# Kernel optimization log

Hardware: AMD Instinct MI355X
Metric: run time of the kernel (lower is better)

## Reference

```python
import jax, jax.numpy as jnp
import numpy as np

NGRAM_NS = (2, 3)  # window sizes of the 2 hidden layers ('2,3,4' -> num_hidden_layers=2)


def _ngram(x, n):
    # x: (b, s, d) -> (b, s, n, d); window i holds x[i:i+n], zero-padded at the end
    s = x.shape[1]
    xp = jnp.pad(x, ((0, 0), (0, n - 1), (0, 0)))
    return jnp.stack([xp[:, j:j + s] for j in range(n)], axis=2)


def _mixture_weighted(r, i, w):
    # r,i: (..., n, d); w: (..., n, 1) -> weighted sum of outer products |phi><phi|
    w = w[..., 0]
    Rr = jnp.einsum('...nd,...ne,...n->...de', r, r, w) + jnp.einsum('...nd,...ne,...n->...de', i, i, w)
    Ri = jnp.einsum('...nd,...ne,...n->...de', i, r, w) - jnp.einsum('...nd,...ne,...n->...de', r, i, w)
    return Rr, Ri


def _normalize_complex(vr, vi):
    n = jnp.sqrt(jnp.sum(vr * vr + vi * vi, axis=-1, keepdims=True))
    return vr / n, vi / n


def _quad_form(Rr, Ri, vr, vi):
    # <v_k| rho |v_k> for each measurement vector v_k; Rr,Ri: (..., d, d); vr,vi: (k, d)
    ar = jnp.einsum('...de,ke->...dk', Rr, vr) - jnp.einsum('...de,ke->...dk', Ri, vi)
    ai = jnp.einsum('...de,ke->...dk', Rr, vi) + jnp.einsum('...de,ke->...dk', Ri, vr)
    out_r = jnp.einsum('kd,...dk->...k', vr, ar) + jnp.einsum('kd,...dk->...k', vi, ai)
    out_i = jnp.einsum('kd,...dk->...k', vr, ai) - jnp.einsum('kd,...dk->...k', vi, ar)
    return out_r, out_i


def setup_inputs() -> dict:
    key = jax.random.key(0)
    ks = jax.random.split(key, 9)
    V, D, B, S, U, L = 50000, 100, 16, 128, 100, 2
    return {
        'input_seq': jax.random.randint(ks[0], (B, S), 0, V),
        'amp_table': jax.random.normal(ks[1], (V, D), jnp.float32),
        'phase_table': jax.random.uniform(ks[2], (V, D), jnp.float32, -np.pi, np.pi),
        'proj_kernel_r': jax.random.normal(ks[3], (L, D, D), jnp.float32),
        'proj_kernel_i': jax.random.normal(ks[4], (L, D, D), jnp.float32),
        'meas_kernel_r': jax.random.normal(ks[5], (U, D), jnp.float32),
        'meas_kernel_i': jax.random.normal(ks[6], (U, D), jnp.float32),
        'dense_w': jax.random.normal(ks[7], (U, 2), jnp.float32) * 0.1,
        'dense_b': jnp.zeros((2,), jnp.float32),
    }


def reference(input_seq, amp_table, phase_table, proj_kernel_r, proj_kernel_i,
              meas_kernel_r, meas_kernel_i, dense_w, dense_b):
    # ComplexEmbedding
    amp = amp_table[input_seq]      # (b, s, d)
    phase = phase_table[input_seq]  # (b, s, d)
    # L2Norm / L2Normalization
    weights = jnp.linalg.norm(amp, axis=-1, keepdims=True)  # (b, s, 1)
    amp = amp / weights
    # ComplexMultiply: state = amp * e^{i phase}
    seq_r = amp * jnp.cos(phase)
    seq_i = amp * jnp.sin(phase)
    for li, n in enumerate(NGRAM_NS):
        gr = _ngram(seq_r, n)                                  # (b, s, n, d)
        gi = _ngram(seq_i, n)
        gw = jax.nn.softmax(_ngram(weights, n), axis=1)        # Softmax(dim=1) as in torch code
        Rr, Ri = _mixture_weighted(gr, gi, gw)                 # (b, s, d, d)
        vr, vi = _normalize_complex(proj_kernel_r[li], proj_kernel_i[li])
        seq_r, seq_i = _quad_form(Rr, Ri, vr, vi)              # (b, s, d)
    # Final mixture over the sequence dim with the raw L2-norm weights
    Rr, Ri = _mixture_weighted(seq_r, seq_i, weights)          # (b, d, d)
    vr, vi = _normalize_complex(meas_kernel_r, meas_kernel_i)
    probs, _ = _quad_form(Rr, Ri, vr, vi)                      # (b, units) real part of Tr(rho P_k)
    return probs @ dense_w + dense_b
```

## Files before the change

kernel.cpp:

```cpp
#include <hip/hip_runtime.h>
#include <math.h>

#define NB 16
#define SS 128
#define DD 100
#define KK 100
#define T_TILE 8
#define NTILES 16
#define NT 768

__device__ __forceinline__ float dot4(const float4 a, const float4 b) {
  return a.x * b.x + a.y * b.y + a.z * b.z + a.w * b.w;
}

template<int MODE, int CM, int NA, int NB2>
__device__ __forceinline__ void do_stage(
    const float* __restrict__ gvr, const float* __restrict__ gvi,
    const float4 (*__restrict__ xR)[25], const float4 (*__restrict__ xI)[25],
    float4 (*__restrict__ partl)[11][50],
    float2 (*__restrict__ nrmh)[50],
    float* __restrict__ mdst, float2* __restrict__ y3f,
    float* __restrict__ invvnU,
    const float* __restrict__ es, const float* __restrict__ sc,
    int df4, int pmaxF, int pmaxC,
    int k0, bool act, int g, int h, int t0)
{
  const float* vr0 = gvr + k0 * DD + 4 * df4;
  const float* vi0 = gvi + k0 * DD + 4 * df4;
  float acr[4][2] = {{0.f,0.f},{0.f,0.f},{0.f,0.f},{0.f,0.f}};
  float aci[4][2] = {{0.f,0.f},{0.f,0.f},{0.f,0.f},{0.f,0.f}};
  float n0 = 0.f, n1 = 0.f;

  {
    float4 V[NA][2][2];
#pragma unroll
    for (int j = 0; j < NA; ++j) {
      V[j][0][0] = *(const float4*)(vr0 + 4 * j);
      V[j][1][0] = *(const float4*)(vr0 + DD + 4 * j);
      V[j][0][1] = *(const float4*)(vi0 + 4 * j);
      V[j][1][1] = *(const float4*)(vi0 + DD + 4 * j);
    }
#pragma unroll
    for (int j = 0; j < NA; ++j) {
      n0 += dot4(V[j][0][0], V[j][0][0]) + dot4(V[j][0][1], V[j][0][1]);
      n1 += dot4(V[j][1][0], V[j][1][0]) + dot4(V[j][1][1], V[j][1][1]);
    }
#pragma unroll
    for (int e = 0; e < 4; ++e) {
      const int p = 4 * g + e;
      if (p <= pmaxF) {
        const float4* xrow  = &xR[p][df4];
        const float4* xirow = &xI[p][df4];
#pragma unroll
        for (int j = 0; j < NA; ++j) {
          const float4 xr = xrow[j];
          if (MODE == 0) {
            const float4 xi = xirow[j];
            acr[e][0] += dot4(V[j][0][0], xr) + dot4(V[j][0][1], xi);
            aci[e][0] += dot4(V[j][0][0], xi) - dot4(V[j][0][1], xr);
            acr[e][1] += dot4(V[j][1][0], xr) + dot4(V[j][1][1], xi);
            aci[e][1] += dot4(V[j][1][0], xi) - dot4(V[j][1][1], xr);
          } else {
            acr[e][0] += dot4(V[j][0][0], xr);
            aci[e][0] += dot4(V[j][0][1], xr);
            acr[e][1] += dot4(V[j][1][0], xr);
            aci[e][1] += dot4(V[j][1][1], xr);
          }
        }
      }
    }
  }
  {
    float4 V[NB2][2][2];
#pragma unroll
    for (int j = 0; j < NB2; ++j) {
      V[j][0][0] = *(const float4*)(vr0 + 4 * (NA + j));
      V[j][1][0] = *(const float4*)(vr0 + DD + 4 * (NA + j));
      V[j][0][1] = *(const float4*)(vi0 + 4 * (NA + j));
      V[j][1][1] = *(const float4*)(vi0 + DD + 4 * (NA + j));
    }
#pragma unroll
    for (int j = 0; j < NB2; ++j) {
      n0 += dot4(V[j][0][0], V[j][0][0]) + dot4(V[j][0][1], V[j][0][1]);
      n1 += dot4(V[j][1][0], V[j][1][0]) + dot4(V[j][1][1], V[j][1][1]);
    }
#pragma unroll
    for (int e = 0; e < 4; ++e) {
      const int p = 4 * g + e;
      if (p <= pmaxF) {
        const float4* xrow  = &xR[p][df4 + NA];
        const float4* xirow = &xI[p][df4 + NA];
#pragma unroll
        for (int j = 0; j < NB2; ++j) {
          const float4 xr = xrow[j];
          if (MODE == 0) {
            const float4 xi = xirow[j];
            acr[e][0] += dot4(V[j][0][0], xr) + dot4(V[j][0][1], xi);
            aci[e][0] += dot4(V[j][0][0], xi) - dot4(V[j][0][1], xr);
            acr[e][1] += dot4(V[j][1][0], xr) + dot4(V[j][1][1], xi);
            aci[e][1] += dot4(V[j][1][0], xi) - dot4(V[j][1][1], xr);
          } else {
            acr[e][0] += dot4(V[j][0][0], xr);
            aci[e][0] += dot4(V[j][0][1], xr);
            acr[e][1] += dot4(V[j][1][0], xr);
            aci[e][1] += dot4(V[j][1][1], xr);
          }
        }
      }
    }
  }

  const int kp = k0 >> 1;
  if (act) {
#pragma unroll
    for (int e = 0; e < 4; ++e) {
      const int p = 4 * g + e;
      if (p <= pmaxF)
        partl[h][p][kp] = make_float4(acr[e][0], aci[e][0], acr[e][1], aci[e][1]);
    }
    if (g == 0) nrmh[h][kp] = make_float2(n0, n1);
  }
  __syncthreads();

  if (h == 0 && act) {
    const float2 q0 = nrmh[0][kp], q1 = nrmh[1][kp], q2 = nrmh[2][kp], q3 = nrmh[3][kp];
    const float iv0 = 1.f / (q0.x + q1.x + q2.x + q3.x);
    const float iv1 = 1.f / (q0.y + q1.y + q2.y + q3.y);
#pragma unroll
    for (int e = 0; e < 4; ++e) {
      const int p = 4 * g + e;
      if (p <= pmaxC) {
        float4 s  = partl[0][p][kp];
        float4 b1 = partl[1][p][kp], b2 = partl[2][p][kp], b3 = partl[3][p][kp];
        s.x += b1.x + b2.x + b3.x;  s.y += b1.y + b2.y + b3.y;
        s.z += b1.z + b2.z + b3.z;  s.w += b1.w + b2.w + b3.w;
        if (CM == 1) {
          *(float2*)(mdst + p * 100 + k0) =
              make_float2((s.x * s.x + s.y * s.y) * iv0,
                          (s.z * s.z + s.w * s.w) * iv1);
        } else if (CM == 2) {
          float4 u  = partl[0][p + 1][kp];
          float4 c1 = partl[1][p + 1][kp], c2 = partl[2][p + 1][kp], c3 = partl[3][p + 1][kp];
          u.x += c1.x + c2.x + c3.x;  u.y += c1.y + c2.y + c3.y;
          u.z += c1.z + c2.z + c3.z;  u.w += c1.w + c2.w + c3.w;
          const int t = t0 + p;
          const float w0 = es[t] / sc[0];
          const float w1 = es[t + 1] / sc[1];
          const float r0 = w0 * s.x + w1 * u.x, i0 = w0 * s.y + w1 * u.y;
          const float r1 = w0 * s.z + w1 * u.z, i1 = w0 * s.w + w1 * u.w;
          *(float2*)(mdst + p * 100 + k0) =
              make_float2((r0 * r0 + i0 * i0) * iv0, (r1 * r1 + i1 * i1) * iv1);
        } else {
          *(float4*)(y3f + p * 100 + k0) = s;
        }
      }
    }
    if (CM == 3 && g == 0) { invvnU[k0] = iv0; invvnU[k0 + 1] = iv1; }
  }
  __syncthreads();
}

__global__ __launch_bounds__(NT, 3) void k_fused(
    const int* __restrict__ seq,
    const float* __restrict__ ampT, const float* __restrict__ phT,
    const float* __restrict__ pkr, const float* __restrict__ pki,
    const float* __restrict__ mkr, const float* __restrict__ mki,
    float* __restrict__ partg)
{
  __shared__ float4 xbR[11][25];
  __shared__ float4 xbI[11][25];
  __shared__ float4 partl[4][11][50];
  __shared__ float2 y3[10][100];
  __shared__ float2 nrmh[4][50];
  __shared__ float invvnU[KK];
  __shared__ float es[SS + 8];
  __shared__ float wnl[SS];
  __shared__ float redw[2];
  __shared__ float sc[3];

  const int tid  = threadIdx.x;
  const int lane = tid & 63;
  const int wid  = tid >> 6;
  const int h    = wid & 3;
  const int g    = wid >> 2;
  const bool act = lane < 50;
  const int kp   = act ? lane : 49;
  const int k0   = 2 * kp;
  const int df4  = (h == 0) ? 0 : 7 + 6 * (h - 1);
  const int bt   = blockIdx.x;
  const int b    = bt >> 4;
  const int t0   = (bt & 15) * T_TILE;
  const int sb   = b * SS;

  if (tid < 512) {
    const int t = tid >> 2, qq = tid & 3;
    const int row = seq[sb + t];
    const float* ap = ampT + (long)row * DD;
    float s = 0.f;
#pragma unroll
    for (int i = 0; i < 7; ++i) {
      const int j = qq + 4 * i;
      if (j < 25) {
        const float4 a = *(const float4*)(ap + 4 * j);
        s += a.x * a.x + a.y * a.y + a.z * a.z + a.w * a.w;
      }
    }
    s += __shfl_xor(s, 1);
    s += __shfl_xor(s, 2);
    if (qq == 0) { const float n = sqrtf(s); wnl[t] = n; es[t] = expf(n); }
  }
  if (tid >= 512 && tid < 520) es[SS + tid - 512] = 0.f;
  __syncthreads();

  if (tid < SS) {
    float v = es[tid];
#pragma unroll
    for (int m = 32; m; m >>= 1) v += __shfl_xor(v, m);
    if ((tid & 63) == 0) redw[tid >> 6] = v;
  }
  for (int e2 = tid; e2 < 11 * DD; e2 += NT) {
    const int p = e2 / DD, d = e2 - p * DD;
    const int t = t0 + p;
    float pr = 0.f, pi = 0.f;
    if (t < SS) {
      const int row = seq[sb + t];
      const float a  = ampT[(long)row * DD + d];
      const float ph = phT[(long)row * DD + d];
      float sv, cv; sincosf(ph, &sv, &cv);
      const float an = a / wnl[t];
      pr = an * cv; pi = an * sv;
    }
    ((float*)xbR)[p * 100 + d] = pr;
    ((float*)xbI)[p * 100 + d] = pi;
  }
  __syncthreads();
  if (tid == 0) {
    const float E = redw[0] + redw[1];
    sc[0] = E; sc[1] = E - es[0] + 1.f; sc[2] = E - es[0] - es[1] + 2.f;
  }
  __syncthreads();

  if (h == 0) do_stage<0,1,4,3>(pkr, pki, xbR, xbI, partl, nrmh,
                                (float*)xbR, nullptr, invvnU, es, sc,
                                0,   10, 10, k0, act, g, h, t0);
  else        do_stage<0,1,3,3>(pkr, pki, xbR, xbI, partl, nrmh,
                                (float*)xbR, nullptr, invvnU, es, sc,
                                df4, 10, 10, k0, act, g, h, t0);

  if (h == 0) do_stage<1,2,4,3>(pkr + DD * DD, pki + DD * DD, xbR, xbI, partl, nrmh,
                                (float*)xbI, nullptr, invvnU, es, sc,
                                0,   10, 9, k0, act, g, h, t0);
  else        do_stage<1,2,3,3>(pkr + DD * DD, pki + DD * DD, xbR, xbI, partl, nrmh,
                                (float*)xbI, nullptr, invvnU, es, sc,
                                df4, 10, 9, k0, act, g, h, t0);

  if (h == 0) do_stage<1,3,4,3>(mkr, mki, xbI, xbI, partl, nrmh,
                                nullptr, (float2*)y3, invvnU, es, sc,
                                0,   9, 9, k0, act, g, h, t0);
  else        do_stage<1,3,3,3>(mkr, mki, xbI, xbI, partl, nrmh,
                                nullptr, (float2*)y3, invvnU, es, sc,
                                df4, 9, 9, k0, act, g, h, t0);

  if (tid < KK) {
    const int k = tid;
    const float iE = 1.f / sc[0], iZ1 = 1.f / sc[1], iZ2 = 1.f / sc[2];
    float acc = 0.f;
#pragma unroll
    for (int p = 0; p < T_TILE; ++p) {
      const int t = t0 + p;
      const float w0 = es[t] * iE;
      const float w1 = es[t + 1] * iZ1;
      const float w2 = es[t + 2] * iZ2;
      const float2 a = y3[p][k], bb = y3[p + 1][k], c = y3[p + 2][k];
      const float qr = w0 * a.x + w1 * bb.x + w2 * c.x;
      const float qi = w0 * a.y + w1 * bb.y + w2 * c.y;
      acc += wnl[t] * (qr * qr + qi * qi);
    }
    partg[bt * KK + k] = acc * invvnU[k];
  }
}

__global__ __launch_bounds__(128) void k_out(
    const float* __restrict__ partg, const float* __restrict__ dw,
    const float* __restrict__ db, float* __restrict__ out)
{
  __shared__ float pr[KK];
  const int b = blockIdx.x, tid = threadIdx.x;
  if (tid < KK) {
    float s = 0.f;
#pragma unroll
    for (int q = 0; q < NTILES; ++q) s += partg[(b * NTILES + q) * KK + tid];
    pr[tid] = s;
  }
  __syncthreads();
  if (tid < 2) {
    float s = db[tid];
    for (int k = 0; k < KK; ++k) s += pr[k] * dw[k * 2 + tid];
    out[b * 2 + tid] = s;
  }
}

extern "C" void kernel_launch(void* const* d_in, const int* in_sizes, int n_in,
                              void* d_out, int out_size, void* d_ws, size_t ws_size,
                              hipStream_t stream) {
  const int*   seq  = (const int*)d_in[0];
  const float* ampT = (const float*)d_in[1];
  const float* phT  = (const float*)d_in[2];
  const float* pkr  = (const float*)d_in[3];
  const float* pki  = (const float*)d_in[4];
  const float* mkr  = (const float*)d_in[5];
  const float* mki  = (const float*)d_in[6];
  const float* dw   = (const float*)d_in[7];
  const float* db   = (const float*)d_in[8];
  float* out   = (float*)d_out;
  float* partg = (float*)d_ws;

  k_fused<<<NB * NTILES, NT, 0, stream>>>(seq, ampT, phT, pkr, pki, mkr, mki, partg);
  k_out  <<<NB,          128, 0, stream>>>(partg, dw, db, out);
}
```

Before: 37.85 us.

## Stage projection vectors via async global-to-LDS loads and split norm kernel

Projection and measurement vectors are now staged into shared memory with global_load_lds using a rotated layout, then read per thread, where before each thread loaded them directly from global memory. The per-sequence norm and softmax statistics move into a separate k_norm kernel, so each fused block no longer recomputes them. The block shrinks from 768 to 512 threads, with each wave group covering six positions instead of four. The change adds a kernel launch and extra barriers per stage, and the shared buffer is reused for partial sums.

```diff
diff --git a/kernel.cpp b/kernel.cpp
--- a/kernel.cpp
+++ b/kernel.cpp
@@ -7,175 +7,205 @@
 #define KK 100
 #define T_TILE 8
 #define NTILES 16
-#define NT 768
+#define NT 512
 
 __device__ __forceinline__ float dot4(const float4 a, const float4 b) {
   return a.x * b.x + a.y * b.y + a.z * b.z + a.w * b.w;
 }
 
-template<int MODE, int CM, int NA, int NB2>
+__device__ __forceinline__ int div25(int x) { return (x * 10486) >> 18; }
+
+__device__ __forceinline__ void stage_part(const float* __restrict__ gv,
+                                           char* vs, int wid, int lane) {
+#pragma unroll
+  for (int ii = 0; ii < 5; ++ii) {
+    const int i = wid + 8 * ii;
+    const int L = (i << 6) + lane;
+    const int k = div25(L);
+    const int s = L - 25 * k;
+    int t = s + 150 - 3 * (k >> 1);
+    t -= 25 * div25(t);
+    const float* src = gv + k * DD + 4 * t;
+    __builtin_amdgcn_global_load_lds(src, (float*)(vs + (i << 10)), 16, 0, 0);
+  }
+}
+
+template<int MODE, int CM>
 __device__ __forceinline__ void do_stage(
     const float* __restrict__ gvr, const float* __restrict__ gvi,
-    const float4 (*__restrict__ xR)[25], const float4 (*__restrict__ xI)[25],
-    float4 (*__restrict__ partl)[11][50],
-    float2 (*__restrict__ nrmh)[50],
-    float* __restrict__ mdst, float2* __restrict__ y3f,
-    float* __restrict__ invvnU,
+    char* vs, const float* __restrict__ xR, const float* __restrict__ xI,
+    float* __restrict__ outp, float* __restrict__ invvnU,
     const float* __restrict__ es, const float* __restrict__ sc,
-    int df4, int pmaxF, int pmaxC,
-    int k0, bool act, int g, int h, int t0)
+    int nu, int O, int pmaxF, int pmaxC,
+    int wid, int lane, int h, int g, int kp, bool act, int t0)
 {
-  const float* vr0 = gvr + k0 * DD + 4 * df4;
-  const float* vi0 = gvi + k0 * DD + 4 * df4;
-  float acr[4][2] = {{0.f,0.f},{0.f,0.f},{0.f,0.f},{0.f,0.f}};
-  float aci[4][2] = {{0.f,0.f},{0.f,0.f},{0.f,0.f},{0.f,0.f}};
+  float4* partlp = (float4*)vs;
+  float2* nrmhp  = (float2*)(vs + 35200);
+  float4 Vr0[7], Vr1[7], Vi0[7], Vi1[7];
   float n0 = 0.f, n1 = 0.f;
 
-  {
-    float4 V[NA][2][2];
-#pragma unroll
-    for (int j = 0; j < NA; ++j) {
-      V[j][0][0] = *(const float4*)(vr0 + 4 * j);
-      V[j][1][0] = *(const float4*)(vr0 + DD + 4 * j);
-      V[j][0][1] = *(const float4*)(vi0 + 4 * j);
-      V[j][1][1] = *(const float4*)(vi0 + DD + 4 * j);
-    }
-#pragma unroll
-    for (int j = 0; j < NA; ++j) {
-      n0 += dot4(V[j][0][0], V[j][0][0]) + dot4(V[j][0][1], V[j][0][1]);
-      n1 += dot4(V[j][1][0], V[j][1][0]) + dot4(V[j][1][1], V[j][1][1]);
-    }
-#pragma unroll
-    for (int e = 0; e < 4; ++e) {
-      const int p = 4 * g + e;
+  const int s3 = 3 * kp;
+  const int sb = (s3 - 25 * div25(s3)) + O;
+
+  stage_part(gvr, vs, wid, lane);
+  __syncthreads();
+#pragma unroll
+  for (int U = 0; U < 7; ++U) if (U < nu) {
+    int su = sb + U; if (su >= 25) su -= 25;
+    const float4* pR = (const float4*)(vs + ((50 * kp + su) << 4));
+    Vr0[U] = pR[0];
+    Vr1[U] = pR[25];
+    n0 += dot4(Vr0[U], Vr0[U]);
+    n1 += dot4(Vr1[U], Vr1[U]);
+  }
+  __syncthreads();
+  stage_part(gvi, vs, wid, lane);
+  __syncthreads();
+#pragma unroll
+  for (int U = 0; U < 7; ++U) if (U < nu) {
+    int su = sb + U; if (su >= 25) su -= 25;
+    const float4* pR = (const float4*)(vs + ((50 * kp + su) << 4));
+    Vi0[U] = pR[0];
+    Vi1[U] = pR[25];
+    n0 += dot4(Vi0[U], Vi0[U]);
+    n1 += dot4(Vi1[U], Vi1[U]);
+  }
+
+  float ar[6][2] = {{0}}, ai[6][2] = {{0}};
+#pragma unroll
+  for (int U = 0; U < 7; ++U) if (U < nu) {
+    const int u = O + U;
+#pragma unroll
+    for (int e = 0; e < 6; ++e) {
+      const int p = 6 * g + e;
       if (p <= pmaxF) {
-        const float4* xrow  = &xR[p][df4];
-        const float4* xirow = &xI[p][df4];
-#pragma unroll
-        for (int j = 0; j < NA; ++j) {
-          const float4 xr = xrow[j];
-          if (MODE == 0) {
-            const float4 xi = xirow[j];
-            acr[e][0] += dot4(V[j][0][0], xr) + dot4(V[j][0][1], xi);
-            aci[e][0] += dot4(V[j][0][0], xi) - dot4(V[j][0][1], xr);
-            acr[e][1] += dot4(V[j][1][0], xr) + dot4(V[j][1][1], xi);
-            aci[e][1] += dot4(V[j][1][0], xi) - dot4(V[j][1][1], xr);
-          } else {
-            acr[e][0] += dot4(V[j][0][0], xr);
-            aci[e][0] += dot4(V[j][0][1], xr);
-            acr[e][1] += dot4(V[j][1][0], xr);
-            aci[e][1] += dot4(V[j][1][1], xr);
-          }
+        const float4 xr = *(const float4*)(xR + p * DD + 4 * u);
+        if (MODE == 0) {
+          const float4 xi = *(const float4*)(xI + p * DD + 4 * u);
+          ar[e][0] += dot4(Vr0[U], xr) + dot4(Vi0[U], xi);
+          ai[e][0] += dot4(Vr0[U], xi) - dot4(Vi0[U], xr);
+          ar[e][1] += dot4(Vr1[U], xr) + dot4(Vi1[U], xi);
+          ai[e][1] += dot4(Vr1[U], xi) - dot4(Vi1[U], xr);
+        } else {
+          ar[e][0] += dot4(Vr0[U], xr);
+          ai[e][0] += dot4(Vi0[U], xr);
+          ar[e][1] += dot4(Vr1[U], xr);
+          ai[e][1] += dot4(Vi1[U], xr);
         }
       }
     }
   }
-  {
-    float4 V[NB2][2][2];
-#pragma unroll
-    for (int j = 0; j < NB2; ++j) {
-      V[j][0][0] = *(const float4*)(vr0 + 4 * (NA + j));
-      V[j][1][0] = *(const float4*)(vr0 + DD + 4 * (NA + j));
-      V[j][0][1] = *(const float4*)(vi0 + 4 * (NA + j));
-      V[j][1][1] = *(const float4*)(vi0 + DD + 4 * (NA + j));
-    }
-#pragma unroll
-    for (int j = 0; j < NB2; ++j) {
-      n0 += dot4(V[j][0][0], V[j][0][0]) + dot4(V[j][0][1], V[j][0][1]);
-      n1 += dot4(V[j][1][0], V[j][1][0]) + dot4(V[j][1][1], V[j][1][1]);
-    }
-#pragma unroll
-    for (int e = 0; e < 4; ++e) {
-      const int p = 4 * g + e;
-      if (p <= pmaxF) {
-        const float4* xrow  = &xR[p][df4 + NA];
-        const float4* xirow = &xI[p][df4 + NA];
-#pragma unroll
-        for (int j = 0; j < NB2; ++j) {
-          const float4 xr = xrow[j];
-          if (MODE == 0) {
-            const float4 xi = xirow[j];
-            acr[e][0] += dot4(V[j][0][0], xr) + dot4(V[j][0][1], xi);
-            aci[e][0] += dot4(V[j][0][0], xi) - dot4(V[j][0][1], xr);
-            acr[e][1] += dot4(V[j][1][0], xr) + dot4(V[j][1][1], xi);
-            aci[e][1] += dot4(V[j][1][0], xi) - dot4(V[j][1][1], xr);
-          } else {
-            acr[e][0] += dot4(V[j][0][0], xr);
-            aci[e][0] += dot4(V[j][0][1], xr);
-            acr[e][1] += dot4(V[j][1][0], xr);
-            aci[e][1] += dot4(V[j][1][1], xr);
-          }
-        }
-      }
-    }
-  }
-
-  const int kp = k0 >> 1;
+  __syncthreads();
+
   if (act) {
 #pragma unroll
-    for (int e = 0; e < 4; ++e) {
-      const int p = 4 * g + e;
+    for (int e = 0; e < 6; ++e) {
+      const int p = 6 * g + e;
       if (p <= pmaxF)
-        partl[h][p][kp] = make_float4(acr[e][0], aci[e][0], acr[e][1], aci[e][1]);
-    }
-    if (g == 0) nrmh[h][kp] = make_float2(n0, n1);
+        partlp[h * 550 + p * 50 + kp] =
+            make_float4(ar[e][0], ai[e][0], ar[e][1], ai[e][1]);
+    }
+    if (g == 0) nrmhp[h * 50 + kp] = make_float2(n0, n1);
   }
   __syncthreads();
 
   if (h == 0 && act) {
-    const float2 q0 = nrmh[0][kp], q1 = nrmh[1][kp], q2 = nrmh[2][kp], q3 = nrmh[3][kp];
+    const float2 q0 = nrmhp[kp], q1 = nrmhp[50 + kp],
+                 q2 = nrmhp[100 + kp], q3 = nrmhp[150 + kp];
     const float iv0 = 1.f / (q0.x + q1.x + q2.x + q3.x);
     const float iv1 = 1.f / (q0.y + q1.y + q2.y + q3.y);
-#pragma unroll
-    for (int e = 0; e < 4; ++e) {
-      const int p = 4 * g + e;
+    const float iZ0 = 1.f / sc[0], iZ1 = 1.f / sc[1];
+#pragma unroll
+    for (int e = 0; e < 6; ++e) {
+      const int p = 6 * g + e;
       if (p <= pmaxC) {
-        float4 s  = partl[0][p][kp];
-        float4 b1 = partl[1][p][kp], b2 = partl[2][p][kp], b3 = partl[3][p][kp];
-        s.x += b1.x + b2.x + b3.x;  s.y += b1.y + b2.y + b3.y;
-        s.z += b1.z + b2.z + b3.z;  s.w += b1.w + b2.w + b3.w;
+        float4 s = partlp[p * 50 + kp];
+        {
+          const float4 b1 = partlp[550 + p * 50 + kp];
+          const float4 b2 = partlp[1100 + p * 50 + kp];
+          const float4 b3 = partlp[1650 + p * 50 + kp];
+          s.x += b1.x + b2.x + b3.x;  s.y += b1.y + b2.y + b3.y;
+          s.z += b1.z + b2.z + b3.z;  s.w += b1.w + b2.w + b3.w;
+        }
         if (CM == 1) {
-          *(float2*)(mdst + p * 100 + k0) =
+          *(float2*)(outp + p * DD + 2 * kp) =
               make_float2((s.x * s.x + s.y * s.y) * iv0,
                           (s.z * s.z + s.w * s.w) * iv1);
         } else if (CM == 2) {
-          float4 u  = partl[0][p + 1][kp];
-          float4 c1 = partl[1][p + 1][kp], c2 = partl[2][p + 1][kp], c3 = partl[3][p + 1][kp];
-          u.x += c1.x + c2.x + c3.x;  u.y += c1.y + c2.y + c3.y;
-          u.z += c1.z + c2.z + c3.z;  u.w += c1.w + c2.w + c3.w;
+          float4 u4 = partlp[(p + 1) * 50 + kp];
+          const float4 c1 = partlp[550 + (p + 1) * 50 + kp];
+          const float4 c2 = partlp[1100 + (p + 1) * 50 + kp];
+          const float4 c3 = partlp[1650 + (p + 1) * 50 + kp];
+          u4.x += c1.x + c2.x + c3.x;  u4.y += c1.y + c2.y + c3.y;
+          u4.z += c1.z + c2.z + c3.z;  u4.w += c1.w + c2.w + c3.w;
           const int t = t0 + p;
-          const float w0 = es[t] / sc[0];
-          const float w1 = es[t + 1] / sc[1];
-          const float r0 = w0 * s.x + w1 * u.x, i0 = w0 * s.y + w1 * u.y;
-          const float r1 = w0 * s.z + w1 * u.z, i1 = w0 * s.w + w1 * u.w;
-          *(float2*)(mdst + p * 100 + k0) =
+          const float w0 = es[t] * iZ0;
+          const float w1 = es[t + 1] * iZ1;
+          const float r0 = w0 * s.x + w1 * u4.x, i0 = w0 * s.y + w1 * u4.y;
+          const float r1 = w0 * s.z + w1 * u4.z, i1 = w0 * s.w + w1 * u4.w;
+          *(float2*)(outp + p * DD + 2 * kp) =
               make_float2((r0 * r0 + i0 * i0) * iv0, (r1 * r1 + i1 * i1) * iv1);
         } else {
-          *(float4*)(y3f + p * 100 + k0) = s;
+          *(float4*)((float2*)outp + p * DD + 2 * kp) = s;
         }
       }
     }
-    if (CM == 3 && g == 0) { invvnU[k0] = iv0; invvnU[k0 + 1] = iv1; }
-  }
-  __syncthreads();
-}
-
-__global__ __launch_bounds__(NT, 3) void k_fused(
+    if (CM == 3 && g == 0) { invvnU[2 * kp] = iv0; invvnU[2 * kp + 1] = iv1; }
+  }
+  __syncthreads();
+}
+
+__global__ __launch_bounds__(512) void k_norm(
+    const int* __restrict__ seq, const float* __restrict__ ampT,
+    float* __restrict__ es_g, float* __restrict__ wnl_g, float* __restrict__ sc_g)
+{
+  __shared__ float esl[SS], wnll[SS], red2[2];
+  const int b = blockIdx.x, tid = threadIdx.x;
+  const int t = tid >> 2, qq = tid & 3;
+  const int row = seq[b * SS + t];
+  const float* ap = ampT + (long)row * DD;
+  float s = 0.f;
+#pragma unroll
+  for (int i = 0; i < 7; ++i) {
+    const int j = qq + 4 * i;
+    if (j < 25) {
+      const float4 a4 = *(const float4*)(ap + 4 * j);
+      s += dot4(a4, a4);
+    }
+  }
+  s += __shfl_xor(s, 1);
+  s += __shfl_xor(s, 2);
+  if (qq == 0) { const float n = sqrtf(s); wnll[t] = n; esl[t] = expf(n); }
+  __syncthreads();
+  if (tid < SS) {
+    float v = esl[tid];
+#pragma unroll
+    for (int m = 32; m; m >>= 1) v += __shfl_xor(v, m);
+    if ((tid & 63) == 0) red2[tid >> 6] = v;
+  }
+  __syncthreads();
+  if (tid < SS) { es_g[b * SS + tid] = esl[tid]; wnl_g[b * SS + tid] = wnll[tid]; }
+  if (tid == 0) {
+    const float E = red2[0] + red2[1];
+    sc_g[b * 4 + 0] = E;
+    sc_g[b * 4 + 1] = E - esl[0] + 1.f;
+    sc_g[b * 4 + 2] = E - esl[0] - esl[1] + 2.f;
+  }
+}
+
+__global__ __launch_bounds__(NT) void k_fused(
     const int* __restrict__ seq,
     const float* __restrict__ ampT, const float* __restrict__ phT,
     const float* __restrict__ pkr, const float* __restrict__ pki,
     const float* __restrict__ mkr, const float* __restrict__ mki,
-    float* __restrict__ partg)
+    const float* __restrict__ es_g, const float* __restrict__ wnl_g,
+    const float* __restrict__ sc_g, float* __restrict__ partg)
 {
-  __shared__ float4 xbR[11][25];
-  __shared__ float4 xbI[11][25];
-  __shared__ float4 partl[4][11][50];
-  __shared__ float2 y3[10][100];
-  __shared__ float2 nrmh[4][50];
-  __shared__ float invvnU[KK];
+  __shared__ __align__(16) char vspace[40960];
+  __shared__ float xb[2200];
   __shared__ float es[SS + 8];
   __shared__ float wnl[SS];
-  __shared__ float redw[2];
+  __shared__ float invvnU[KK];
   __shared__ float sc[3];
 
   const int tid  = threadIdx.x;
@@ -185,39 +215,21 @@
   const int g    = wid >> 2;
   const bool act = lane < 50;
   const int kp   = act ? lane : 49;
-  const int k0   = 2 * kp;
-  const int df4  = (h == 0) ? 0 : 7 + 6 * (h - 1);
   const int bt   = blockIdx.x;
   const int b    = bt >> 4;
   const int t0   = (bt & 15) * T_TILE;
   const int sb   = b * SS;
-
-  if (tid < 512) {
-    const int t = tid >> 2, qq = tid & 3;
-    const int row = seq[sb + t];
-    const float* ap = ampT + (long)row * DD;
-    float s = 0.f;
-#pragma unroll
-    for (int i = 0; i < 7; ++i) {
-      const int j = qq + 4 * i;
-      if (j < 25) {
-        const float4 a = *(const float4*)(ap + 4 * j);
-        s += a.x * a.x + a.y * a.y + a.z * a.z + a.w * a.w;
-      }
-    }
-    s += __shfl_xor(s, 1);
-    s += __shfl_xor(s, 2);
-    if (qq == 0) { const float n = sqrtf(s); wnl[t] = n; es[t] = expf(n); }
-  }
-  if (tid >= 512 && tid < 520) es[SS + tid - 512] = 0.f;
-  __syncthreads();
-
-  if (tid < SS) {
-    float v = es[tid];
-#pragma unroll
-    for (int m = 32; m; m >>= 1) v += __shfl_xor(v, m);
-    if ((tid & 63) == 0) redw[tid >> 6] = v;
-  }
+  const int O    = (h == 0) ? 0 : 7 + 6 * (h - 1);
+  const int nu   = (h == 0) ? 7 : 6;
+
+  float* xbR = xb;
+  float* xbI = xb + 1100;
+
+  if (tid < SS) { es[tid] = es_g[sb + tid]; wnl[tid] = wnl_g[sb + tid]; }
+  if (tid >= SS && tid < SS + 8) es[tid] = 0.f;
+  if (tid < 3) sc[tid] = sc_g[(b << 2) + tid];
+  __syncthreads();
+
   for (int e2 = tid; e2 < 11 * DD; e2 += NT) {
     const int p = e2 / DD, d = e2 - p * DD;
     const int t = t0 + p;
@@ -230,38 +242,20 @@
       const float an = a / wnl[t];
       pr = an * cv; pi = an * sv;
     }
-    ((float*)xbR)[p * 100 + d] = pr;
-    ((float*)xbI)[p * 100 + d] = pi;
-  }
-  __syncthreads();
-  if (tid == 0) {
-    const float E = redw[0] + redw[1];
-    sc[0] = E; sc[1] = E - es[0] + 1.f; sc[2] = E - es[0] - es[1] + 2.f;
-  }
-  __syncthreads();
-
-  if (h == 0) do_stage<0,1,4,3>(pkr, pki, xbR, xbI, partl, nrmh,
-                                (float*)xbR, nullptr, invvnU, es, sc,
-                                0,   10, 10, k0, act, g, h, t0);
-  else        do_stage<0,1,3,3>(pkr, pki, xbR, xbI, partl, nrmh,
-                                (float*)xbR, nullptr, invvnU, es, sc,
-                                df4, 10, 10, k0, act, g, h, t0);
-
-  if (h == 0) do_stage<1,2,4,3>(pkr + DD * DD, pki + DD * DD, xbR, xbI, partl, nrmh,
-                                (float*)xbI, nullptr, invvnU, es, sc,
-                                0,   10, 9, k0, act, g, h, t0);
-  else        do_stage<1,2,3,3>(pkr + DD * DD, pki + DD * DD, xbR, xbI, partl, nrmh,
-                                (float*)xbI, nullptr, invvnU, es, sc,
-                                df4, 10, 9, k0, act, g, h, t0);
-
-  if (h == 0) do_stage<1,3,4,3>(mkr, mki, xbI, xbI, partl, nrmh,
-                                nullptr, (float2*)y3, invvnU, es, sc,
-                                0,   9, 9, k0, act, g, h, t0);
-  else        do_stage<1,3,3,3>(mkr, mki, xbI, xbI, partl, nrmh,
-                                nullptr, (float2*)y3, invvnU, es, sc,
-                                df4, 9, 9, k0, act, g, h, t0);
+    xbR[p * DD + d] = pr;
+    xbI[p * DD + d] = pi;
+  }
+  __syncthreads();
+
+  do_stage<0, 1>(pkr, pki, vspace, xbR, xbI, xbR, invvnU, es, sc,
+                 nu, O, 10, 10, wid, lane, h, g, kp, act, t0);
+  do_stage<1, 2>(pkr + DD * DD, pki + DD * DD, vspace, xbR, xbR, xbI, invvnU,
+                 es, sc, nu, O, 10, 9, wid, lane, h, g, kp, act, t0);
+  do_stage<1, 3>(mkr, mki, vspace, xbI, xbI, xb, invvnU, es, sc,
+                 nu, O, 9, 9, wid, lane, h, g, kp, act, t0);
 
   if (tid < KK) {
+    const float2* y3f = (const float2*)xb;
     const int k = tid;
     const float iE = 1.f / sc[0], iZ1 = 1.f / sc[1], iZ2 = 1.f / sc[2];
     float acc = 0.f;
@@ -271,7 +265,8 @@
       const float w0 = es[t] * iE;
       const float w1 = es[t + 1] * iZ1;
       const float w2 = es[t + 2] * iZ2;
-      const float2 a = y3[p][k], bb = y3[p + 1][k], c = y3[p + 2][k];
+      const float2 a = y3f[p * DD + k], bb = y3f[(p + 1) * DD + k],
+                   c = y3f[(p + 2) * DD + k];
       const float qr = w0 * a.x + w1 * bb.x + w2 * c.x;
       const float qi = w0 * a.y + w1 * bb.y + w2 * c.y;
       acc += wnl[t] * (qr * qr + qi * qi);
@@ -312,9 +307,16 @@
   const float* mki  = (const float*)d_in[6];
   const float* dw   = (const float*)d_in[7];
   const float* db   = (const float*)d_in[8];
-  float* out   = (float*)d_out;
-  float* partg = (float*)d_ws;
-
-  k_fused<<<NB * NTILES, NT, 0, stream>>>(seq, ampT, phT, pkr, pki, mkr, mki, partg);
+  float* out = (float*)d_out;
+
+  float* ws    = (float*)d_ws;
+  float* es_g  = ws;
+  float* wnl_g = ws + 2048;
+  float* sc_g  = ws + 4096;
+  float* partg = ws + 4160;
+
+  k_norm <<<NB,          512, 0, stream>>>(seq, ampT, es_g, wnl_g, sc_g);
+  k_fused<<<NB * NTILES, NT,  0, stream>>>(seq, ampT, phT, pkr, pki, mkr, mki,
+                                           es_g, wnl_g, sc_g, partg);
   k_out  <<<NB,          128, 0, stream>>>(partg, dw, db, out);
 }
```

Measured after the change: 138.8 us. 3.67x slower.
